# Kernel optimization log

Hardware: AMD Instinct MI355X
Metric: run time of the kernel (lower is better)

Reference implementation:

```python
import jax, jax.numpy as jnp
import numpy as np
from jax import lax

EPS = 1e-5
DW_THRESH = 4.0
PW_THRESH = 1e-3


def setup_inputs() -> dict:
    key = jax.random.key(0)
    ks = jax.random.split(key, 13)
    B, C, O, H, W = 32, 256, 256, 56, 56
    inp = {
        "x": jax.random.normal(ks[0], (B, C, H, W), jnp.float32),
        "dw_w": jax.random.normal(ks[1], (C, 1, 3, 3), jnp.float32) * 0.2,
        "dw_b": jax.random.normal(ks[2], (C,), jnp.float32) * 0.1,
        "bn1_gamma": 0.5 + jax.random.uniform(ks[3], (C,), jnp.float32) * 1.5,
        "bn1_beta": jax.random.normal(ks[4], (C,), jnp.float32) * 0.5,
        "bn1_mean": jax.random.normal(ks[5], (C,), jnp.float32) * 0.1,
        "bn1_var": 0.5 + jax.random.uniform(ks[6], (C,), jnp.float32),
        "pw_w": jax.random.normal(ks[7], (O, C, 1, 1), jnp.float32) * 0.06,
        "pw_b": jax.random.normal(ks[8], (O,), jnp.float32) * 0.1,
        "bn2_gamma": 0.5 + jax.random.uniform(ks[9], (O,), jnp.float32) * 1.5,
        "bn2_beta": jax.random.normal(ks[10], (O,), jnp.float32) * 0.5,
        "bn2_mean": jax.random.normal(ks[11], (O,), jnp.float32) * 0.1,
        "bn2_var": 0.5 + jax.random.uniform(ks[12], (O,), jnp.float32),
    }
    return inp


def _bn(x, gamma, beta, mean, var):
    # inference-mode BatchNorm2d over channel axis 1
    inv = gamma * lax.rsqrt(var + EPS)
    return x * inv[None, :, None, None] + (beta - mean * inv)[None, :, None, None]


def _cut(x, thresh):
    # per-(batch, channel) max-abs pruning: max(max(x), -min(x)) == max(|x|)
    max_abs = jnp.max(jnp.abs(x), axis=(2, 3))  # [B, C]
    return jnp.where((max_abs < thresh)[:, :, None, None], 0.0, x)


def reference(x, dw_w, dw_b, bn1_gamma, bn1_beta, bn1_mean, bn1_var,
              pw_w, pw_b, bn2_gamma, bn2_beta, bn2_mean, bn2_var):
    C = x.shape[1]
    # depthwise 3x3 conv, padding=1, groups=C
    y = lax.conv_general_dilated(
        x, dw_w, window_strides=(1, 1), padding=[(1, 1), (1, 1)],
        feature_group_count=C,
        dimension_numbers=("NCHW", "OIHW", "NCHW"),
    ) + dw_b[None, :, None, None]
    y = jax.nn.relu(_bn(y, bn1_gamma, bn1_beta, bn1_mean, bn1_var))
    y = _cut(y, DW_THRESH)
    # pointwise 1x1 conv as channel contraction
    z = jnp.einsum("bihw,oi->bohw", y, pw_w[:, :, 0, 0]) + pw_b[None, :, None, None]
    z = jax.nn.relu(_bn(z, bn2_gamma, bn2_beta, bn2_mean, bn2_var))
    z = _cut(z, PW_THRESH)
    return z
```

## Files before the change

### kernel.cpp

```cpp
#include <hip/hip_runtime.h>
#include <hip/hip_bf16.h>
#include <stdint.h>

#define BATCH 32
#define CIN   256
#define COUT  256
#define HW    3136
#define NPAD  3200

typedef short bf16x8 __attribute__((ext_vector_type(8)));
typedef float f32x4  __attribute__((ext_vector_type(4)));

__device__ __forceinline__ unsigned short f2bf(float f) {
    unsigned u = __float_as_uint(f);
    u += 0x7fffu + ((u >> 16) & 1u);
    return (unsigned short)(u >> 16);
}

__global__ __launch_bounds__(256) void prep_kernel(
        const float* __restrict__ pw_w, const float* __restrict__ pw_b,
        const float* __restrict__ g2, const float* __restrict__ be2,
        const float* __restrict__ mu2, const float* __restrict__ va2,
        unsigned short* __restrict__ Wp, float* __restrict__ b2,
        unsigned* __restrict__ pwmax) {
    int o = blockIdx.x;
    int t = threadIdx.x;
    float inv2 = g2[o] * rsqrtf(va2[o] + 1e-5f);
    Wp[o * CIN + t] = f2bf(pw_w[o * CIN + t] * inv2);
    if (t == 0) b2[o] = pw_b[o] * inv2 + be2[o] - mu2[o] * inv2;
    int idx = blockIdx.x * 256 + t;
    if (idx < BATCH * COUT) pwmax[idx] = 0u;
}

__global__ __launch_bounds__(256) void dw_kernel(
        const float* __restrict__ x, const float* __restrict__ dww,
        const float* __restrict__ dwb,
        const float* __restrict__ g1, const float* __restrict__ be1,
        const float* __restrict__ mu1, const float* __restrict__ va1,
        unsigned short* __restrict__ y, float* __restrict__ dwmax) {
    int lane = threadIdx.x & 63;
    int wid  = threadIdx.x >> 6;
    int plane = blockIdx.x * 4 + wid;
    int c = plane & 255;

    int col = lane < 56 ? lane : 55;
    bool active = lane < 56;
    const float* xp = x + (size_t)plane * HW + col;
    unsigned short* yp = y + (size_t)plane * NPAD + col;

    float w00 = dww[c*9+0], w01 = dww[c*9+1], w02 = dww[c*9+2];
    float w10 = dww[c*9+3], w11 = dww[c*9+4], w12 = dww[c*9+5];
    float w20 = dww[c*9+6], w21 = dww[c*9+7], w22 = dww[c*9+8];
    float inv = g1[c] * rsqrtf(va1[c] + 1e-5f);
    float b0  = dwb[c] * inv + (be1[c] - mu1[c] * inv);

    float A = 0.f;
    float B = 0.f;
    float lmax = 0.f;

#pragma unroll
    for (int q = 0; q < 56; ++q) {
        float xv = xp[q * 56];
        float xl = __shfl_up(xv, 1, 64);
        float xr = __shfl_down(xv, 1, 64);
        if (lane == 0)  xl = 0.f;
        if (lane >= 55) xr = 0.f;
        float outv = fmaf(xl, w20, fmaf(xv, w21, fmaf(xr, w22, A)));
        A = fmaf(xl, w10, fmaf(xv, w11, fmaf(xr, w12, B)));
        B = fmaf(xl, w00, fmaf(xv, w01, xr * w02));
        if (q >= 1) {
            float v = fmaxf(fmaf(outv, inv, b0), 0.f);
            if (active) {
                lmax = fmaxf(lmax, v);
                yp[(q - 1) * 56] = f2bf(v);
            }
        }
    }
    {
        float v = fmaxf(fmaf(A, inv, b0), 0.f);
        if (active) {
            lmax = fmaxf(lmax, v);
            yp[55 * 56] = f2bf(v);
        }
    }
    for (int off = 32; off >= 1; off >>= 1)
        lmax = fmaxf(lmax, __shfl_xor(lmax, off, 64));
    if (lane == 0) dwmax[plane] = lmax;
    if (lane < 8) *(uint4*)(y + (size_t)plane * NPAD + HW + lane * 8)
        = make_uint4(0, 0, 0, 0);
}

__global__ __launch_bounds__(256) void pw_kernel(
        const unsigned short* __restrict__ y, const unsigned short* __restrict__ Wp,
        const float* __restrict__ b2, const float* __restrict__ dwm,
        float* __restrict__ z, unsigned* __restrict__ pwmax) {
    __shared__ __align__(16) unsigned short Al[128 * 64];
    __shared__ __align__(16) unsigned short Bl[128 * 64];

    int bid0 = blockIdx.x;
    int bid = (bid0 & 7) * 200 + (bid0 >> 3);
    int mt = bid & 1;
    int rest = bid >> 1;
    int nt = rest % 25;
    int b = rest / 25;
    int m0 = mt * 128, n0 = nt * 128;

    int tid = threadIdx.x;
    int lane = tid & 63, wid = tid >> 6;
    int wm = (wid & 1) * 64, wn = (wid >> 1) * 64;
    int l15 = lane & 15, l4 = lane >> 4;

    const unsigned short* yb = y + (size_t)b * CIN * NPAD;
    const float* dwb_ = dwm + b * 256;

    int am[4], acch[4];
    const unsigned short* asrc[4];
#pragma unroll
    for (int i = 0; i < 4; ++i) {
        int s = i * 256 + tid;
        int m = s >> 3, cch = s & 7, dch = cch ^ (m & 7);
        am[i] = m; acch[i] = cch;
        asrc[i] = Wp + (size_t)(m0 + m) * CIN + dch * 8;
    }
    int bq[2], bnq[2];
    const unsigned short* bsrc[2];
#pragma unroll
    for (int i = 0; i < 2; ++i) {
        int u = tid + i * 256;
        bq[i] = u >> 5; bnq[i] = u & 31;
        bsrc[i] = yb + (size_t)(bq[i] * 4) * NPAD + n0 + bnq[i] * 4;
    }

    uint4 areg[4];
    uint2 breg[2][4];
    float4 fl[2];
#pragma unroll
    for (int i = 0; i < 4; ++i) areg[i] = *(const uint4*)(asrc[i]);
#pragma unroll
    for (int i = 0; i < 2; ++i) {
#pragma unroll
        for (int r = 0; r < 4; ++r) breg[i][r] = *(const uint2*)(bsrc[i] + r * NPAD);
        fl[i] = *(const float4*)(dwb_ + bq[i] * 4);
    }

    f32x4 acc[4][4];
#pragma unroll
    for (int mf = 0; mf < 4; ++mf)
#pragma unroll
        for (int nf = 0; nf < 4; ++nf) acc[mf][nf] = {0.f, 0.f, 0.f, 0.f};

#pragma unroll
    for (int kk = 0; kk < 4; ++kk) {
        __builtin_amdgcn_s_barrier();
        __builtin_amdgcn_sched_barrier(0);
#pragma unroll
        for (int i = 0; i < 4; ++i)
            *(uint4*)((char*)Al + am[i] * 128 + acch[i] * 16) = areg[i];
#pragma unroll
        for (int i = 0; i < 2; ++i) {
            unsigned mk0 = fl[i].x >= 4.0f ? 0xffffffffu : 0u;
            unsigned mk1 = fl[i].y >= 4.0f ? 0xffffffffu : 0u;
            unsigned mk2 = fl[i].z >= 4.0f ? 0xffffffffu : 0u;
            unsigned mk3 = fl[i].w >= 4.0f ? 0xffffffffu : 0u;
            uint2 r0 = breg[i][0], r1 = breg[i][1], r2 = breg[i][2], r3 = breg[i][3];
            r0.x &= mk0; r0.y &= mk0; r1.x &= mk1; r1.y &= mk1;
            r2.x &= mk2; r2.y &= mk2; r3.x &= mk3; r3.y &= mk3;
            int q = bq[i], nq = bnq[i];
#pragma unroll
            for (int i2 = 0; i2 < 4; ++i2) {
                unsigned x0 = (i2 & 2) ? r0.y : r0.x;
                unsigned x1 = (i2 & 2) ? r1.y : r1.x;
                unsigned x2 = (i2 & 2) ? r2.y : r2.x;
                unsigned x3 = (i2 & 2) ? r3.y : r3.x;
                if (i2 & 1) { x0 >>= 16; x2 >>= 16; }
                else        { x0 &= 0xffffu; x2 &= 0xffffu; }
                unsigned px = (i2 & 1) ? (x0 | (x1 & 0xffff0000u))
                                       : (x0 | (x1 << 16));
                unsigned py = (i2 & 1) ? (x2 | (x3 & 0xffff0000u))
                                       : (x2 | (x3 << 16));
                int nloc = nq * 4 + i2;
                int sb = nloc * 128 + (((q >> 1) ^ ((nloc >> 2) & 7)) << 4) + ((q & 1) << 3);
                *(uint2*)((char*)Bl + sb) = make_uint2(px, py);
            }
        }
        if (kk < 3) {
#pragma unroll
            for (int i = 0; i < 4; ++i)
                areg[i] = *(const uint4*)(asrc[i] + (kk + 1) * 64);
#pragma unroll
            for (int i = 0; i < 2; ++i) {
#pragma unroll
                for (int r = 0; r < 4; ++r)
                    breg[i][r] = *(const uint2*)(bsrc[i] + (size_t)(kk + 1) * 64 * NPAD + r * NPAD);
                fl[i] = *(const float4*)(dwb_ + (kk + 1) * 64 + bq[i] * 4);
            }
        }
        asm volatile("s_waitcnt lgkmcnt(0)" ::: "memory");
        __builtin_amdgcn_s_barrier();
        __builtin_amdgcn_sched_barrier(0);
#pragma unroll
        for (int h = 0; h < 2; ++h) {
            bf16x8 af[4], bfr[4];
            int cc = h * 4 + l4;
#pragma unroll
            for (int mf = 0; mf < 4; ++mf) {
                int m = wm + mf * 16 + l15;
                af[mf] = *(const bf16x8*)((const char*)Al + m * 128 + ((cc ^ (m & 7)) << 4));
            }
#pragma unroll
            for (int nf = 0; nf < 4; ++nf) {
                int n = wn + nf * 16 + l15;
                bfr[nf] = *(const bf16x8*)((const char*)Bl + n * 128 + ((cc ^ ((n >> 2) & 7)) << 4));
            }
#pragma unroll
            for (int mf = 0; mf < 4; ++mf)
#pragma unroll
                for (int nf = 0; nf < 4; ++nf)
                    acc[mf][nf] = __builtin_amdgcn_mfma_f32_16x16x32_bf16(
                        af[mf], bfr[nf], acc[mf][nf], 0, 0, 0);
        }
    }

    float* zb = z + (size_t)b * COUT * HW;
#pragma unroll
    for (int mf = 0; mf < 4; ++mf) {
        int obase = m0 + wm + mf * 16 + l4 * 4;
        float bb0 = b2[obase + 0], bb1 = b2[obase + 1];
        float bb2v = b2[obase + 2], bb3 = b2[obase + 3];
        float rmax[4] = {0.f, 0.f, 0.f, 0.f};
#pragma unroll
        for (int nf = 0; nf < 4; ++nf) {
            int n = n0 + wn + nf * 16 + l15;
            bool valid = (n < HW);
            float v0 = fmaxf(acc[mf][nf][0] + bb0, 0.f);
            float v1 = fmaxf(acc[mf][nf][1] + bb1, 0.f);
            float v2 = fmaxf(acc[mf][nf][2] + bb2v, 0.f);
            float v3 = fmaxf(acc[mf][nf][3] + bb3, 0.f);
            if (valid) {
                zb[(size_t)(obase + 0) * HW + n] = v0;
                zb[(size_t)(obase + 1) * HW + n] = v1;
                zb[(size_t)(obase + 2) * HW + n] = v2;
                zb[(size_t)(obase + 3) * HW + n] = v3;
                rmax[0] = fmaxf(rmax[0], v0);
                rmax[1] = fmaxf(rmax[1], v1);
                rmax[2] = fmaxf(rmax[2], v2);
                rmax[3] = fmaxf(rmax[3], v3);
            }
        }
#pragma unroll
        for (int r = 0; r < 4; ++r) {
            float v = rmax[r];
            v = fmaxf(v, __shfl_xor(v, 1, 64));
            v = fmaxf(v, __shfl_xor(v, 2, 64));
            v = fmaxf(v, __shfl_xor(v, 4, 64));
            v = fmaxf(v, __shfl_xor(v, 8, 64));
            if (l15 == 0)
                atomicMax(&pwmax[b * COUT + obase + r], __float_as_uint(v));
        }
    }
}

__global__ __launch_bounds__(256) void cut_kernel(const unsigned* __restrict__ pwmax,
                                                  float* __restrict__ z) {
    int base = blockIdx.x * 8;
#pragma unroll
    for (int j = 0; j < 8; ++j) {
        int bo = base + j;
        if (__uint_as_float(pwmax[bo]) >= 1e-3f) continue;
        float4* zp = (float4*)(z + (size_t)bo * HW);
        for (int i = threadIdx.x; i < HW / 4; i += 256)
            zp[i] = make_float4(0.f, 0.f, 0.f, 0.f);
    }
}

extern "C" void kernel_launch(void* const* d_in, const int* in_sizes, int n_in,
                              void* d_out, int out_size, void* d_ws, size_t ws_size,
                              hipStream_t stream) {
    const float* x   = (const float*)d_in[0];
    const float* dww = (const float*)d_in[1];
    const float* dwb = (const float*)d_in[2];
    const float* g1  = (const float*)d_in[3];
    const float* be1 = (const float*)d_in[4];
    const float* mu1 = (const float*)d_in[5];
    const float* va1 = (const float*)d_in[6];
    const float* pww = (const float*)d_in[7];
    const float* pwb = (const float*)d_in[8];
    const float* g2  = (const float*)d_in[9];
    const float* be2 = (const float*)d_in[10];
    const float* mu2 = (const float*)d_in[11];
    const float* va2 = (const float*)d_in[12];
    float* z = (float*)d_out;

    char* ws = (char*)d_ws;
    const size_t Y_BYTES = (size_t)BATCH * CIN * NPAD * 2;
    unsigned short* y  = (unsigned short*)ws;
    unsigned short* Wp = (unsigned short*)(ws + Y_BYTES);
    float* b2          = (float*)(ws + Y_BYTES + 131072);
    unsigned* pwmax    = (unsigned*)(ws + Y_BYTES + 131072 + 1024);
    float* dwmax       = (float*)(ws + Y_BYTES + 131072 + 1024 + 32768);

    prep_kernel<<<256, 256, 0, stream>>>(pww, pwb, g2, be2, mu2, va2, Wp, b2, pwmax);
    dw_kernel<<<2048, 256, 0, stream>>>(x, dww, dwb, g1, be1, mu1, va1, y, dwmax);
    pw_kernel<<<1600, 256, 0, stream>>>(y, Wp, b2, dwmax, z, pwmax);
    cut_kernel<<<BATCH * COUT / 8, 256, 0, stream>>>(pwmax, z);
}
```

Before: 110.6 us.

## Stage dw input via global_load_lds and prefetch all K-steps in pw GEMM

The depthwise kernel now loads each full input plane into shared memory with direct global-to-LDS loads, then reads the left, center and right neighbours from LDS instead of using cross-lane shuffles. It processes two rows per iteration, and boundary handling is moved into zeroed weights. The pointwise GEMM loads the whole 128x256 weight tile into LDS at the start with async global_load_lds. It also issues all four K-step B loads into registers up front, gated by staged vmcnt waits, and adds launch bounds for 2 blocks per CU. This is meant to hide global-load latency, but it raises LDS use (64KB A tile plus B) and register pressure, which may limit occupancy.

```diff
diff --git a/kernel.cpp b/kernel.cpp
--- a/kernel.cpp
+++ b/kernel.cpp
@@ -7,6 +7,9 @@
 #define COUT  256
 #define HW    3136
 #define NPAD  3200
+
+#define AS1 __attribute__((address_space(1)))
+#define AS3 __attribute__((address_space(3)))
 
 typedef short bf16x8 __attribute__((ext_vector_type(8)));
 typedef float f32x4  __attribute__((ext_vector_type(4)));
@@ -38,15 +41,23 @@
         const float* __restrict__ g1, const float* __restrict__ be1,
         const float* __restrict__ mu1, const float* __restrict__ va1,
         unsigned short* __restrict__ y, float* __restrict__ dwmax) {
-    int lane = threadIdx.x & 63;
-    int wid  = threadIdx.x >> 6;
+    __shared__ float xs[4 * 3136];
+    int tid  = threadIdx.x;
+    int lane = tid & 63, wid = tid >> 6;
     int plane = blockIdx.x * 4 + wid;
     int c = plane & 255;
 
-    int col = lane < 56 ? lane : 55;
-    bool active = lane < 56;
-    const float* xp = x + (size_t)plane * HW + col;
-    unsigned short* yp = y + (size_t)plane * NPAD + col;
+    const float* xp = x + (size_t)plane * HW;
+    float* xw = xs + wid * 3136;
+
+#pragma unroll
+    for (int i = 0; i < 12; ++i)
+        __builtin_amdgcn_global_load_lds(
+            (const AS1 void*)(xp + i * 256 + lane * 4),
+            (AS3 void*)(xw + i * 256), 16, 0, 0);
+    __builtin_amdgcn_global_load_lds(
+        (const AS1 void*)(xp + 3072 + lane),
+        (AS3 void*)(xw + 3072), 4, 0, 0);
 
     float w00 = dww[c*9+0], w01 = dww[c*9+1], w02 = dww[c*9+2];
     float w10 = dww[c*9+3], w11 = dww[c*9+4], w12 = dww[c*9+5];
@@ -54,34 +65,44 @@
     float inv = g1[c] * rsqrtf(va1[c] + 1e-5f);
     float b0  = dwb[c] * inv + (be1[c] - mu1[c] * inv);
 
+    int  col    = lane < 56 ? lane : 55;
+    bool active = lane < 56;
+    if (lane == 0)  { w00 = 0.f; w10 = 0.f; w20 = 0.f; }
+    if (lane >= 55) { w02 = 0.f; w12 = 0.f; w22 = 0.f; }
+    int il = (lane == 0) ? 0 : col - 1;
+    int ir = (col == 55) ? 55 : col + 1;
+
+    asm volatile("s_waitcnt vmcnt(0)" ::: "memory");
+    __builtin_amdgcn_sched_barrier(0);
+
+    const float* xb = xw;
+    unsigned short* yp = y + (size_t)plane * NPAD + col;
+
     float A = 0.f;
-    float B = 0.f;
+    float Bv = 0.f;
     float lmax = 0.f;
-
-#pragma unroll
-    for (int q = 0; q < 56; ++q) {
-        float xv = xp[q * 56];
-        float xl = __shfl_up(xv, 1, 64);
-        float xr = __shfl_down(xv, 1, 64);
-        if (lane == 0)  xl = 0.f;
-        if (lane >= 55) xr = 0.f;
-        float outv = fmaf(xl, w20, fmaf(xv, w21, fmaf(xr, w22, A)));
-        A = fmaf(xl, w10, fmaf(xv, w11, fmaf(xr, w12, B)));
-        B = fmaf(xl, w00, fmaf(xv, w01, xr * w02));
-        if (q >= 1) {
-            float v = fmaxf(fmaf(outv, inv, b0), 0.f);
-            if (active) {
-                lmax = fmaxf(lmax, v);
-                yp[(q - 1) * 56] = f2bf(v);
-            }
-        }
+#pragma unroll
+    for (int q = 0; q < 56; q += 2) {
+        float l0 = xb[q*56 + il],      c0 = xb[q*56 + col],      r0 = xb[q*56 + ir];
+        float l1 = xb[(q+1)*56 + il],  c1 = xb[(q+1)*56 + col],  r1 = xb[(q+1)*56 + ir];
+        if (q > 0) {
+            float o0 = fmaf(l0, w20, fmaf(c0, w21, fmaf(r0, w22, A)));
+            float v = fmaxf(fmaf(o0, inv, b0), 0.f);
+            if (active) { lmax = fmaxf(lmax, v); yp[(q-1)*56] = f2bf(v); }
+        }
+        {
+            float o1 = fmaf(l0, w10, fmaf(c0, w11, fmaf(r0, w12,
+                       fmaf(l1, w20, fmaf(c1, w21, fmaf(r1, w22, Bv))))));
+            float v = fmaxf(fmaf(o1, inv, b0), 0.f);
+            if (active) { lmax = fmaxf(lmax, v); yp[q*56] = f2bf(v); }
+        }
+        float top0 = fmaf(l0, w00, fmaf(c0, w01, r0 * w02));
+        A  = fmaf(l1, w10, fmaf(c1, w11, fmaf(r1, w12, top0)));
+        Bv = fmaf(l1, w00, fmaf(c1, w01, r1 * w02));
     }
     {
         float v = fmaxf(fmaf(A, inv, b0), 0.f);
-        if (active) {
-            lmax = fmaxf(lmax, v);
-            yp[55 * 56] = f2bf(v);
-        }
+        if (active) { lmax = fmaxf(lmax, v); yp[55*56] = f2bf(v); }
     }
     for (int off = 32; off >= 1; off >>= 1)
         lmax = fmaxf(lmax, __shfl_xor(lmax, off, 64));
@@ -90,11 +111,11 @@
         = make_uint4(0, 0, 0, 0);
 }
 
-__global__ __launch_bounds__(256) void pw_kernel(
+__global__ __launch_bounds__(256, 2) void pw_kernel(
         const unsigned short* __restrict__ y, const unsigned short* __restrict__ Wp,
         const float* __restrict__ b2, const float* __restrict__ dwm,
         float* __restrict__ z, unsigned* __restrict__ pwmax) {
-    __shared__ __align__(16) unsigned short Al[128 * 64];
+    __shared__ __align__(16) unsigned short Al[128 * 256];
     __shared__ __align__(16) unsigned short Bl[128 * 64];
 
     int bid0 = blockIdx.x;
@@ -113,14 +134,12 @@
     const unsigned short* yb = y + (size_t)b * CIN * NPAD;
     const float* dwb_ = dwm + b * 256;
 
-    int am[4], acch[4];
-    const unsigned short* asrc[4];
-#pragma unroll
-    for (int i = 0; i < 4; ++i) {
-        int s = i * 256 + tid;
+    const unsigned short* agsrc[4];
+#pragma unroll
+    for (int ii = 0; ii < 4; ++ii) {
+        int s = ii * 256 + wid * 64 + lane;
         int m = s >> 3, cch = s & 7, dch = cch ^ (m & 7);
-        am[i] = m; acch[i] = cch;
-        asrc[i] = Wp + (size_t)(m0 + m) * CIN + dch * 8;
+        agsrc[ii] = Wp + (size_t)(m0 + m) * CIN + dch * 8;
     }
     int bq[2], bnq[2];
     const unsigned short* bsrc[2];
@@ -131,16 +150,29 @@
         bsrc[i] = yb + (size_t)(bq[i] * 4) * NPAD + n0 + bnq[i] * 4;
     }
 
-    uint4 areg[4];
-    uint2 breg[2][4];
-    float4 fl[2];
-#pragma unroll
-    for (int i = 0; i < 4; ++i) areg[i] = *(const uint4*)(asrc[i]);
-#pragma unroll
-    for (int i = 0; i < 2; ++i) {
-#pragma unroll
-        for (int r = 0; r < 4; ++r) breg[i][r] = *(const uint2*)(bsrc[i] + r * NPAD);
-        fl[i] = *(const float4*)(dwb_ + bq[i] * 4);
+#pragma unroll
+    for (int ks = 0; ks < 4; ++ks)
+#pragma unroll
+        for (int ii = 0; ii < 4; ++ii)
+            __builtin_amdgcn_global_load_lds(
+                (const AS1 void*)(agsrc[ii] + ks * 64),
+                (AS3 void*)((char*)Al + ks * 16384 + ii * 4096 + wid * 1024),
+                16, 0, 0);
+    __builtin_amdgcn_sched_barrier(0);
+
+    uint2 breg[4][2][4];
+    float4 fl[4][2];
+#pragma unroll
+    for (int kk = 0; kk < 4; ++kk) {
+#pragma unroll
+        for (int i = 0; i < 2; ++i)
+#pragma unroll
+            for (int r = 0; r < 4; ++r)
+                breg[kk][i][r] = *(const uint2*)(bsrc[i] + (size_t)kk * 64 * NPAD + r * NPAD);
+#pragma unroll
+        for (int i = 0; i < 2; ++i)
+            fl[kk][i] = *(const float4*)(dwb_ + kk * 64 + bq[i] * 4);
+        __builtin_amdgcn_sched_barrier(0);
     }
 
     f32x4 acc[4][4];
@@ -151,18 +183,19 @@
 
 #pragma unroll
     for (int kk = 0; kk < 4; ++kk) {
-        __builtin_amdgcn_s_barrier();
+        if (kk == 0) asm volatile("s_waitcnt vmcnt(30)" ::: "memory");
+        if (kk == 1) asm volatile("s_waitcnt vmcnt(20)" ::: "memory");
+        if (kk == 2) asm volatile("s_waitcnt vmcnt(10)" ::: "memory");
+        if (kk == 3) asm volatile("s_waitcnt vmcnt(0)"  ::: "memory");
         __builtin_amdgcn_sched_barrier(0);
 #pragma unroll
-        for (int i = 0; i < 4; ++i)
-            *(uint4*)((char*)Al + am[i] * 128 + acch[i] * 16) = areg[i];
-#pragma unroll
         for (int i = 0; i < 2; ++i) {
-            unsigned mk0 = fl[i].x >= 4.0f ? 0xffffffffu : 0u;
-            unsigned mk1 = fl[i].y >= 4.0f ? 0xffffffffu : 0u;
-            unsigned mk2 = fl[i].z >= 4.0f ? 0xffffffffu : 0u;
-            unsigned mk3 = fl[i].w >= 4.0f ? 0xffffffffu : 0u;
-            uint2 r0 = breg[i][0], r1 = breg[i][1], r2 = breg[i][2], r3 = breg[i][3];
+            unsigned mk0 = fl[kk][i].x >= 4.0f ? 0xffffffffu : 0u;
+            unsigned mk1 = fl[kk][i].y >= 4.0f ? 0xffffffffu : 0u;
+            unsigned mk2 = fl[kk][i].z >= 4.0f ? 0xffffffffu : 0u;
+            unsigned mk3 = fl[kk][i].w >= 4.0f ? 0xffffffffu : 0u;
+            uint2 r0 = breg[kk][i][0], r1 = breg[kk][i][1];
+            uint2 r2 = breg[kk][i][2], r3 = breg[kk][i][3];
             r0.x &= mk0; r0.y &= mk0; r1.x &= mk1; r1.y &= mk1;
             r2.x &= mk2; r2.y &= mk2; r3.x &= mk3; r3.y &= mk3;
             int q = bq[i], nq = bnq[i];
@@ -183,18 +216,6 @@
                 *(uint2*)((char*)Bl + sb) = make_uint2(px, py);
             }
         }
-        if (kk < 3) {
-#pragma unroll
-            for (int i = 0; i < 4; ++i)
-                areg[i] = *(const uint4*)(asrc[i] + (kk + 1) * 64);
-#pragma unroll
-            for (int i = 0; i < 2; ++i) {
-#pragma unroll
-                for (int r = 0; r < 4; ++r)
-                    breg[i][r] = *(const uint2*)(bsrc[i] + (size_t)(kk + 1) * 64 * NPAD + r * NPAD);
-                fl[i] = *(const float4*)(dwb_ + (kk + 1) * 64 + bq[i] * 4);
-            }
-        }
         asm volatile("s_waitcnt lgkmcnt(0)" ::: "memory");
         __builtin_amdgcn_s_barrier();
         __builtin_amdgcn_sched_barrier(0);
@@ -205,12 +226,14 @@
 #pragma unroll
             for (int mf = 0; mf < 4; ++mf) {
                 int m = wm + mf * 16 + l15;
-                af[mf] = *(const bf16x8*)((const char*)Al + m * 128 + ((cc ^ (m & 7)) << 4));
+                af[mf] = *(const bf16x8*)((const char*)Al + kk * 16384
+                             + m * 128 + ((cc ^ (m & 7)) << 4));
             }
 #pragma unroll
             for (int nf = 0; nf < 4; ++nf) {
                 int n = wn + nf * 16 + l15;
-                bfr[nf] = *(const bf16x8*)((const char*)Bl + n * 128 + ((cc ^ ((n >> 2) & 7)) << 4));
+                bfr[nf] = *(const bf16x8*)((const char*)Bl + n * 128
+                             + ((cc ^ ((n >> 2) & 7)) << 4));
             }
 #pragma unroll
             for (int mf = 0; mf < 4; ++mf)
@@ -219,6 +242,7 @@
                     acc[mf][nf] = __builtin_amdgcn_mfma_f32_16x16x32_bf16(
                         af[mf], bfr[nf], acc[mf][nf], 0, 0, 0);
         }
+        __builtin_amdgcn_s_barrier();
     }
 
     float* zb = z + (size_t)b * COUT * HW;
```

Result: faster. 100.8 us (-8.9%).
